# Kernel optimization log

Measured on AMD Instinct MI355X. Metric: run time of the kernel, lower is better.

The kernel has to match this reference:

```python
import jax, jax.numpy as jnp
import numpy as np

N_HEAD = 16
HEAD_SIZE = 64  # n_embd // n_head = 1024 // 16


def setup_inputs() -> dict:
    key = jax.random.key(0)
    k1, k2 = jax.random.split(key)
    B, T, C = 2, 2048, 1024
    x = jax.random.normal(k1, (B, T, C), dtype=jnp.float32)
    w_attn = jax.random.normal(k2, (C, 3 * C), dtype=jnp.float32) * (C ** -0.5)
    b_attn = jnp.zeros((3 * C,), dtype=jnp.float32)
    return {"x": x, "w_attn": w_attn, "b_attn": b_attn}


def reference(x, w_attn, b_attn):
    B, T, C = x.shape
    qkv = x @ w_attn + b_attn  # [B, T, 3C]
    q, k, v = jnp.split(qkv, 3, axis=-1)
    # [B, T, H, D] -> [B, H, T, D]
    def heads(t):
        return t.reshape(B, T, N_HEAD, HEAD_SIZE).transpose(0, 2, 1, 3)
    q, k, v = heads(q), heads(k), heads(v)
    scale = HEAD_SIZE ** -0.5
    wei = jnp.einsum('bhqd,bhkd->bhqk', q, k) * scale  # [B, H, T, T]
    causal = jnp.tril(jnp.ones((T, T), dtype=bool))
    wei = jnp.where(causal, wei, -jnp.inf)
    wei = jax.nn.softmax(wei, axis=-1)
    out = jnp.einsum('bhqk,bhkd->bhqd', wei, v)  # [B, H, T, D]
    out = out.transpose(0, 2, 1, 3).reshape(B, T, C)
    return out
```

## Files before the change

kernel.cpp:

```cpp
#include <hip/hip_runtime.h>
#include <hip/hip_bf16.h>

#define BSZ 2
#define SEQ 2048
#define CDIM 1024
#define NHEAD 16
#define HDIM 64
#define M_GEMM (BSZ * SEQ)
#define N_GEMM (3 * CDIM)
#define K_GEMM CDIM
#define QK_PITCH (2 * CDIM)

typedef __attribute__((ext_vector_type(8))) short short8;
typedef __attribute__((ext_vector_type(4))) short short4v;
typedef __attribute__((ext_vector_type(4))) float f32x4;

__device__ __forceinline__ short bf16_rn(float f) {
    unsigned u = __builtin_bit_cast(unsigned, f);
    u += 0x7FFF + ((u >> 16) & 1);
    return (short)(u >> 16);
}

__device__ __forceinline__ void gl2lds16(const short* g, short* l) {
    __builtin_amdgcn_global_load_lds(
        (const __attribute__((address_space(1))) unsigned int*)g,
        (__attribute__((address_space(3))) unsigned int*)l, 16, 0, 0);
}

__global__ __launch_bounds__(256) void cvt_fused(const float* __restrict__ X,
                                                 const float* __restrict__ W,
                                                 short* __restrict__ Xb,
                                                 short* __restrict__ WT) {
    const int tid = threadIdx.x;
    if (blockIdx.x < 2048) {
        size_t idx = ((size_t)blockIdx.x * 256 + tid) * 8;
        float4 a = *(const float4*)&X[idx];
        float4 b = *(const float4*)&X[idx + 4];
        short8 o;
        o[0] = bf16_rn(a.x); o[1] = bf16_rn(a.y); o[2] = bf16_rn(a.z); o[3] = bf16_rn(a.w);
        o[4] = bf16_rn(b.x); o[5] = bf16_rn(b.y); o[6] = bf16_rn(b.z); o[7] = bf16_rn(b.w);
        *(short8*)&Xb[idx] = o;
        return;
    }
    __shared__ short T[64][72];
    const int bid = blockIdx.x - 2048;
    const int n0 = (bid % 48) * 64;
    const int k0 = (bid / 48) * 64;
#pragma unroll
    for (int pass = 0; pass < 4; ++pass) {
        int i = pass * 256 + tid;
        int kr = i >> 4;
        int n4 = i & 15;
        float4 v = *(const float4*)&W[(size_t)(k0 + kr) * N_GEMM + n0 + n4 * 4];
        T[n4 * 4 + 0][kr] = bf16_rn(v.x);
        T[n4 * 4 + 1][kr] = bf16_rn(v.y);
        T[n4 * 4 + 2][kr] = bf16_rn(v.z);
        T[n4 * 4 + 3][kr] = bf16_rn(v.w);
    }
    __syncthreads();
#pragma unroll
    for (int pass = 0; pass < 2; ++pass) {
        int o = pass * 256 + tid;
        int nr = o >> 3;
        int c8 = o & 7;
        *(short8*)&WT[(size_t)(n0 + nr) * K_GEMM + k0 + c8 * 8] =
            *(const short8*)&T[nr][c8 * 8];
    }
}

#define GBK 64

__global__ __launch_bounds__(256) void qkv_gemm_mfma(const short* __restrict__ A,
                                                     const short* __restrict__ Bt,
                                                     const float* __restrict__ bias,
                                                     short* __restrict__ Yqk,
                                                     short* __restrict__ Yv) {
    __shared__ short Asl[128 * GBK];
    __shared__ short Bsl[128 * GBK];

    const int tid = threadIdx.x;
    const int w = tid >> 6;
    const int l16 = tid & 15;
    const int quad = (tid & 63) >> 4;
    const int wm = w >> 1, wn = w & 1;
    const int m0 = blockIdx.y * 128;
    const int n0 = blockIdx.x * 128;

    f32x4 acc[4][4];
#pragma unroll
    for (int i = 0; i < 4; ++i)
#pragma unroll
        for (int j = 0; j < 4; ++j) acc[i][j] = (f32x4){0.f, 0.f, 0.f, 0.f};

    int arow[4], gofs[4];
#pragma unroll
    for (int p = 0; p < 4; ++p) {
        int cid = p * 256 + tid;
        arow[p] = cid >> 3;
        gofs[p] = ((cid & 7) ^ (arow[p] & 7)) * 8;
    }
    const int fsw = l16 & 7;

    for (int kt = 0; kt < K_GEMM; kt += GBK) {
        __syncthreads();
#pragma unroll
        for (int p = 0; p < 4; ++p) {
            gl2lds16(A + (size_t)(m0 + arow[p]) * K_GEMM + kt + gofs[p],
                     &Asl[(p * 256 + w * 64) * 8]);
            gl2lds16(Bt + (size_t)(n0 + arow[p]) * K_GEMM + kt + gofs[p],
                     &Bsl[(p * 256 + w * 64) * 8]);
        }
        __syncthreads();

        short8 af[4][2], bfr[4][2];
#pragma unroll
        for (int i = 0; i < 4; ++i) {
            int ra = wm * 64 + i * 16 + l16;
            int rb = wn * 64 + i * 16 + l16;
#pragma unroll
            for (int ks = 0; ks < 2; ++ks) {
                af[i][ks] = *(const short8*)&Asl[(ra * 8 + ((ks * 4 + quad) ^ fsw)) * 8];
                bfr[i][ks] = *(const short8*)&Bsl[(rb * 8 + ((ks * 4 + quad) ^ fsw)) * 8];
            }
        }
#pragma unroll
        for (int i = 0; i < 4; ++i)
#pragma unroll
            for (int j = 0; j < 4; ++j)
#pragma unroll
                for (int ks = 0; ks < 2; ++ks)
                    acc[i][j] = __builtin_amdgcn_mfma_f32_16x16x32_bf16(
                        af[i][ks], bfr[j][ks], acc[i][j], 0, 0, 0);
    }

    if (n0 >= 2 * CDIM) {
#pragma unroll
        for (int i = 0; i < 4; ++i) {
            int row0 = m0 + wm * 64 + i * 16 + quad * 4;
#pragma unroll
            for (int j = 0; j < 4; ++j) {
                int colg = n0 + wn * 64 + j * 16 + l16;
                float bb = bias[colg];
                short4v pk;
#pragma unroll
                for (int r = 0; r < 4; ++r) pk[r] = bf16_rn(acc[i][j][r] + bb);
                *(short4v*)&Yv[(size_t)(colg - 2 * CDIM) * M_GEMM + row0] = pk;
            }
        }
    } else {
        const float qs = (n0 < CDIM) ? 0.125f : 1.0f;
#pragma unroll
        for (int i = 0; i < 4; ++i)
#pragma unroll
            for (int r = 0; r < 4; ++r) {
                int row = m0 + wm * 64 + i * 16 + quad * 4 + r;
#pragma unroll
                for (int j = 0; j < 4; ++j) {
                    int colg = n0 + wn * 64 + j * 16 + l16;
                    Yqk[(size_t)row * QK_PITCH + colg] =
                        bf16_rn((acc[i][j][r] + bias[colg]) * qs);
                }
            }
    }
}

__global__ __launch_bounds__(256) void attn_mfma(const short* __restrict__ qk,
                                                 const short* __restrict__ vT,
                                                 float* __restrict__ out) {
    const int b = blockIdx.z;
    const int h = blockIdx.y;
    const int bx = blockIdx.x;
    const int u = h + 16 * b;
    const int band = u >> 3;
    const int base = (band & 2) ? ((bx + 16) & 31) : bx;
    const int qt = (band & 1) ? (31 - base) : base;
    const int tid = threadIdx.x;
    const int w = tid >> 6;
    const int lane = tid & 63;
    const int quad = lane >> 4;
    const int l16 = lane & 15;
    const int q0 = qt * 64;

    __shared__ short Ks[2][64 * 64];
    __shared__ short Vt[2][64 * 64];
    __shared__ short Ps[4 * 16 * 64];

    int koff[2], voff[2], ldso[2];
#pragma unroll
    for (int p = 0; p < 2; ++p) {
        int cid = p * 256 + w * 64 + lane;
        int row = cid >> 3;
        int c = (cid & 7) ^ (row & 7);
        koff[p] = row * QK_PITCH + c * 8;
        voff[p] = row * M_GEMM + c * 8;
        ldso[p] = (p * 256 + w * 64) * 8;
    }

    const short* qrow = qk + (size_t)(b * SEQ + q0 + w * 16 + l16) * QK_PITCH + h * HDIM;
    short8 aq[2];
    aq[0] = *(const short8*)(qrow + quad * 8);
    aq[1] = *(const short8*)(qrow + 32 + quad * 8);

    float l_run[4] = {0.f, 0.f, 0.f, 0.f};
    f32x4 o_acc[4];
#pragma unroll
    for (int dt = 0; dt < 4; ++dt) o_acc[dt] = (f32x4){0.f, 0.f, 0.f, 0.f};

    const int rowg0 = q0 + w * 16 + quad * 4;
    const short* kb0 = qk + (size_t)(b * SEQ) * QK_PITCH + CDIM + h * HDIM;
    const short* vb0 = vT + (size_t)(h * HDIM) * M_GEMM + b * SEQ;

    const int ksl = l16 & 7;
    short* PsW = &Ps[w * 1024];

#pragma unroll
    for (int p = 0; p < 2; ++p) {
        gl2lds16(kb0 + koff[p], &Ks[0][ldso[p]]);
        gl2lds16(vb0 + voff[p], &Vt[0][ldso[p]]);
    }
    __syncthreads();

    for (int kt = 0; kt <= qt; ++kt) {
        const int cur = kt & 1;

        if (kt < qt) {
            const short* kbase = kb0 + (size_t)(kt + 1) * 64 * QK_PITCH;
            const short* vbase = vb0 + (kt + 1) * 64;
#pragma unroll
            for (int p = 0; p < 2; ++p) {
                gl2lds16(kbase + koff[p], &Ks[cur ^ 1][ldso[p]]);
                gl2lds16(vbase + voff[p], &Vt[cur ^ 1][ldso[p]]);
            }
        }

        const short* KsC = Ks[cur];
        const short* VtC = Vt[cur];

        f32x4 s[4];
#pragma unroll
        for (int nt = 0; nt < 4; ++nt) s[nt] = (f32x4){0.f, 0.f, 0.f, 0.f};
#pragma unroll
        for (int nt = 0; nt < 4; ++nt)
#pragma unroll
            for (int ks = 0; ks < 2; ++ks) {
                short8 bk = *(const short8*)&KsC[(nt * 16 + l16) * 64 +
                                                 ((ks * 4 + quad) ^ ksl) * 8];
                s[nt] = __builtin_amdgcn_mfma_f32_16x16x32_bf16(aq[ks], bk, s[nt], 0, 0, 0);
            }

        if (kt < qt) {
#pragma unroll
            for (int r = 0; r < 4; ++r) {
                const int qr = quad * 4 + r;
                float lsum = 0.f;
#pragma unroll
                for (int nt = 0; nt < 4; ++nt) {
                    float pp = __expf(s[nt][r]);
                    lsum += pp;
                    int slot = (nt * 2 + (l16 >> 3)) ^ (qr & 7);
                    PsW[qr * 64 + slot * 8 + (l16 & 7)] = bf16_rn(pp);
                }
                l_run[r] += lsum;
            }
        } else {
            const int keyb = kt * 64 + l16;
#pragma unroll
            for (int r = 0; r < 4; ++r) {
                const int qr = quad * 4 + r;
                const int rowg = rowg0 + r;
                float lsum = 0.f;
#pragma unroll
                for (int nt = 0; nt < 4; ++nt) {
                    float pp = __expf(s[nt][r]);
                    pp = ((keyb + nt * 16) > rowg) ? 0.f : pp;
                    lsum += pp;
                    int slot = (nt * 2 + (l16 >> 3)) ^ (qr & 7);
                    PsW[qr * 64 + slot * 8 + (l16 & 7)] = bf16_rn(pp);
                }
                l_run[r] += lsum;
            }
        }

#pragma unroll
        for (int dt = 0; dt < 4; ++dt)
#pragma unroll
            for (int ks = 0; ks < 2; ++ks) {
                short8 ap = *(const short8*)&PsW[l16 * 64 + ((ks * 4 + quad) ^ ksl) * 8];
                short8 bv = *(const short8*)&VtC[(dt * 16 + l16) * 64 +
                                                 ((ks * 4 + quad) ^ ksl) * 8];
                o_acc[dt] = __builtin_amdgcn_mfma_f32_16x16x32_bf16(ap, bv, o_acc[dt], 0, 0, 0);
            }

        __syncthreads();
    }

#pragma unroll
    for (int r = 0; r < 4; ++r) {
        float l = l_run[r];
#pragma unroll
        for (int off = 1; off < 16; off <<= 1)
            l += __shfl_xor(l, off);
        float inv = 1.f / l;
        int row = q0 + w * 16 + quad * 4 + r;
        float* optr = out + (size_t)(b * SEQ + row) * CDIM + h * HDIM;
#pragma unroll
        for (int dt = 0; dt < 4; ++dt)
            optr[dt * 16 + l16] = o_acc[dt][r] * inv;
    }
}

extern "C" void kernel_launch(void* const* d_in, const int* in_sizes, int n_in,
                              void* d_out, int out_size, void* d_ws, size_t ws_size,
                              hipStream_t stream) {
    const float* x      = (const float*)d_in[0];
    const float* w_attn = (const float*)d_in[1];
    const float* b_attn = (const float*)d_in[2];
    float* out = (float*)d_out;

    short* qk  = (short*)d_ws;
    short* vT  = (short*)((char*)d_ws + 16777216);
    short* xb  = (short*)((char*)d_ws + 25165824);
    short* wT  = (short*)((char*)d_ws + 33554432);

    cvt_fused<<<2048 + 768, 256, 0, stream>>>(x, w_attn, xb, wT);

    dim3 g1(N_GEMM / 128, M_GEMM / 128);
    qkv_gemm_mfma<<<g1, 256, 0, stream>>>(xb, wT, b_attn, qk, vT);

    dim3 g2(SEQ / 64, NHEAD, BSZ);
    attn_mfma<<<g2, 256, 0, stream>>>(qk, vT, out);
}
```

Before: 168.7 us.

## Double-buffer QKV GEMM LDS tiles and fold log2e into Q scale for exp2

The QKV GEMM now uses a double-buffered LDS tile with half the K depth (32 instead of 64). The next tile's global-to-LDS load is issued before the MFMAs on the current tile, leaving one barrier per iteration instead of two. The swizzle pattern is adapted to the narrower tile. Separately, the Q scale now folds in log2(e), so the attention softmax can use exp2f instead of __expf and drop a multiply per element. The smaller K tile doubles the loop trip count and halves the MFMA work between barriers.

```diff
diff --git a/kernel.cpp b/kernel.cpp
--- a/kernel.cpp
+++ b/kernel.cpp
@@ -68,15 +68,15 @@
     }
 }
 
-#define GBK 64
+#define GBK 32
 
 __global__ __launch_bounds__(256) void qkv_gemm_mfma(const short* __restrict__ A,
                                                      const short* __restrict__ Bt,
                                                      const float* __restrict__ bias,
                                                      short* __restrict__ Yqk,
                                                      short* __restrict__ Yv) {
-    __shared__ short Asl[128 * GBK];
-    __shared__ short Bsl[128 * GBK];
+    __shared__ short Asl[2][128 * GBK];
+    __shared__ short Bsl[2][128 * GBK];
 
     const int tid = threadIdx.x;
     const int w = tid >> 6;
@@ -92,45 +92,52 @@
 #pragma unroll
         for (int j = 0; j < 4; ++j) acc[i][j] = (f32x4){0.f, 0.f, 0.f, 0.f};
 
-    int arow[4], gofs[4];
-#pragma unroll
-    for (int p = 0; p < 4; ++p) {
+    int arow[2], gofs[2], ldso[2];
+#pragma unroll
+    for (int p = 0; p < 2; ++p) {
         int cid = p * 256 + tid;
-        arow[p] = cid >> 3;
-        gofs[p] = ((cid & 7) ^ (arow[p] & 7)) * 8;
-    }
-    const int fsw = l16 & 7;
+        arow[p] = cid >> 2;
+        gofs[p] = ((cid & 3) ^ (arow[p] & 3)) * 8;
+        ldso[p] = (p * 256 + w * 64) * 8;
+    }
+    const int fsw = quad ^ (l16 & 3);
+
+#pragma unroll
+    for (int p = 0; p < 2; ++p) {
+        gl2lds16(A + (size_t)(m0 + arow[p]) * K_GEMM + gofs[p], &Asl[0][ldso[p]]);
+        gl2lds16(Bt + (size_t)(n0 + arow[p]) * K_GEMM + gofs[p], &Bsl[0][ldso[p]]);
+    }
+    __syncthreads();
 
     for (int kt = 0; kt < K_GEMM; kt += GBK) {
-        __syncthreads();
-#pragma unroll
-        for (int p = 0; p < 4; ++p) {
-            gl2lds16(A + (size_t)(m0 + arow[p]) * K_GEMM + kt + gofs[p],
-                     &Asl[(p * 256 + w * 64) * 8]);
-            gl2lds16(Bt + (size_t)(n0 + arow[p]) * K_GEMM + kt + gofs[p],
-                     &Bsl[(p * 256 + w * 64) * 8]);
-        }
-        __syncthreads();
-
-        short8 af[4][2], bfr[4][2];
+        const int cur = (kt >> 5) & 1;
+
+        if (kt + GBK < K_GEMM) {
+#pragma unroll
+            for (int p = 0; p < 2; ++p) {
+                gl2lds16(A + (size_t)(m0 + arow[p]) * K_GEMM + kt + GBK + gofs[p],
+                         &Asl[cur ^ 1][ldso[p]]);
+                gl2lds16(Bt + (size_t)(n0 + arow[p]) * K_GEMM + kt + GBK + gofs[p],
+                         &Bsl[cur ^ 1][ldso[p]]);
+            }
+        }
+
+        short8 af[4], bfr[4];
 #pragma unroll
         for (int i = 0; i < 4; ++i) {
             int ra = wm * 64 + i * 16 + l16;
             int rb = wn * 64 + i * 16 + l16;
-#pragma unroll
-            for (int ks = 0; ks < 2; ++ks) {
-                af[i][ks] = *(const short8*)&Asl[(ra * 8 + ((ks * 4 + quad) ^ fsw)) * 8];
-                bfr[i][ks] = *(const short8*)&Bsl[(rb * 8 + ((ks * 4 + quad) ^ fsw)) * 8];
-            }
+            af[i] = *(const short8*)&Asl[cur][(ra * 4 + fsw) * 8];
+            bfr[i] = *(const short8*)&Bsl[cur][(rb * 4 + fsw) * 8];
         }
 #pragma unroll
         for (int i = 0; i < 4; ++i)
 #pragma unroll
             for (int j = 0; j < 4; ++j)
-#pragma unroll
-                for (int ks = 0; ks < 2; ++ks)
-                    acc[i][j] = __builtin_amdgcn_mfma_f32_16x16x32_bf16(
-                        af[i][ks], bfr[j][ks], acc[i][j], 0, 0, 0);
+                acc[i][j] = __builtin_amdgcn_mfma_f32_16x16x32_bf16(
+                    af[i], bfr[j], acc[i][j], 0, 0, 0);
+
+        __syncthreads();
     }
 
     if (n0 >= 2 * CDIM) {
@@ -148,7 +155,7 @@
             }
         }
     } else {
-        const float qs = (n0 < CDIM) ? 0.125f : 1.0f;
+        const float qs = (n0 < CDIM) ? 0.125f * 1.44269504f : 1.0f;
 #pragma unroll
         for (int i = 0; i < 4; ++i)
 #pragma unroll
@@ -255,7 +262,7 @@
                 float lsum = 0.f;
 #pragma unroll
                 for (int nt = 0; nt < 4; ++nt) {
-                    float pp = __expf(s[nt][r]);
+                    float pp = exp2f(s[nt][r]);
                     lsum += pp;
                     int slot = (nt * 2 + (l16 >> 3)) ^ (qr & 7);
                     PsW[qr * 64 + slot * 8 + (l16 & 7)] = bf16_rn(pp);
@@ -271,7 +278,7 @@
                 float lsum = 0.f;
 #pragma unroll
                 for (int nt = 0; nt < 4; ++nt) {
-                    float pp = __expf(s[nt][r]);
+                    float pp = exp2f(s[nt][r]);
                     pp = ((keyb + nt * 16) > rowg) ? 0.f : pp;
                     lsum += pp;
                     int slot = (nt * 2 + (l16 >> 3)) ^ (qr & 7);
```

New measurement: 190.1 us. 1.13x slower.
